# Performance work log

Hardware: AMD Instinct MI355X
Metric: run time of the kernel (lower is better)

The kernel has to match this reference:

```python
import jax, jax.numpy as jnp
import numpy as np

TEMPERATURE = 0.07
COS_EPS = 1e-8  # torch F.cosine_similarity clamps norms at eps=1e-8


def setup_inputs() -> dict:
    key = jax.random.key(0)
    features = jax.random.normal(key, (8192, 1024), dtype=jnp.float32)
    return {"features": features}


def reference(features):
    n = features.shape[0]
    b = n // 2
    # Cosine similarity as normalize + GEMM (equivalent to broadcasted F.cosine_similarity)
    norms = jnp.maximum(jnp.linalg.norm(features, axis=1, keepdims=True), COS_EPS)
    fn = features / norms                      # [N, D]
    sim = (fn @ fn.T) / TEMPERATURE            # [N, N]
    # Mask self-similarity on the diagonal with -inf
    diag = jnp.eye(n, dtype=bool)
    sim = jnp.where(diag, -jnp.inf, sim)
    # labels: positive of i is its paired augmentation (i+b mod n)
    labels = jnp.concatenate([jnp.arange(b) + b, jnp.arange(b)])  # [N]
    # Cross-entropy in one stable pass
    log_probs = jax.nn.log_softmax(sim, axis=1)
    loss = -jnp.mean(log_probs[jnp.arange(n), labels])
    return loss
```

## Files before the change

kernel.cpp:

```cpp
#include <hip/hip_runtime.h>
#include <hip/hip_bf16.h>

#define N_ROWS 8192
#define D_DIM  1024
#define HALF_N 4096
#define N_TILES 2080
constexpr float INV_T = 1.0f / 0.07f;

typedef __attribute__((ext_vector_type(4))) float f32x4;
typedef unsigned long u64;

__device__ __forceinline__ void async_ld16(const void* g, void* lds) {
    __builtin_amdgcn_global_load_lds(
        (const __attribute__((address_space(1))) void*)g,
        (__attribute__((address_space(3))) void*)lds,
        16, 0, 0);
}

__device__ __forceinline__ unsigned int pk_fp8x4(float a, float b, float c, float d) {
    int v = __builtin_amdgcn_cvt_pk_fp8_f32(a, b, 0, false);
    v = __builtin_amdgcn_cvt_pk_fp8_f32(c, d, v, true);
    return (unsigned int)v;
}

__global__ __launch_bounds__(256) void norm_kernel(const float* __restrict__ feat,
                                                   unsigned char* __restrict__ fn8,
                                                   float* __restrict__ row_sum,
                                                   float* __restrict__ s_target) {
    const int w = threadIdx.x >> 6, lane = threadIdx.x & 63;
    const int row = blockIdx.x * 4 + w;
    const int pair = (row + HALF_N) & (N_ROWS - 1);
    const float4* src = (const float4*)(feat + (size_t)row * D_DIM);
    const float4* psrc = (const float4*)(feat + (size_t)pair * D_DIM);
    float4 v[4];
    float ss = 0.f, sp = 0.f, dp = 0.f;
#pragma unroll
    for (int t = 0; t < 4; ++t) {
        v[t] = src[lane + 64 * t];
        float4 p = psrc[lane + 64 * t];
        ss += v[t].x * v[t].x + v[t].y * v[t].y + v[t].z * v[t].z + v[t].w * v[t].w;
        sp += p.x * p.x + p.y * p.y + p.z * p.z + p.w * p.w;
        dp += v[t].x * p.x + v[t].y * p.y + v[t].z * p.z + v[t].w * p.w;
    }
#pragma unroll
    for (int off = 32; off; off >>= 1) {
        ss += __shfl_xor(ss, off);
        sp += __shfl_xor(sp, off);
        dp += __shfl_xor(dp, off);
    }
    float nrm = fmaxf(sqrtf(ss), 1e-8f);
    if (lane == 0) {
        row_sum[row] = 0.f;
        s_target[row] = dp / (nrm * fmaxf(sqrtf(sp), 1e-8f)) * INV_T;
    }
    const float inv = 1.0f / nrm;
    unsigned int* dst = (unsigned int*)(fn8 + (size_t)row * D_DIM);
#pragma unroll
    for (int t = 0; t < 4; ++t)
        dst[lane + 64 * t] = pk_fp8x4(v[t].x * inv, v[t].y * inv, v[t].z * inv, v[t].w * inv);
}

__global__ __launch_bounds__(256) void simgemm_kernel(const unsigned char* __restrict__ fn8,
                                                      float* __restrict__ row_sum) {
    __shared__ __align__(16) unsigned char As[128 * 64];
    __shared__ __align__(16) unsigned char Bs[128 * 64];
    const int t = blockIdx.x;
    int a = (int)((sqrtf(8.f * (float)t + 1.f) - 1.f) * 0.5f);
    while ((a + 1) * (a + 2) / 2 <= t) ++a;
    while (a * (a + 1) / 2 > t) --a;
    const int I = t - a * (a + 1) / 2;
    const int J = a;
    const int r0 = I * 128, c0 = J * 128;
    const bool isdiag = (I == J);

    const int tid = threadIdx.x;
    const int w = tid >> 6, lane = tid & 63;
    const int q = lane >> 4, c16 = lane & 15;
    const int wr = (w >> 1) * 64;
    const int wc = (w & 1) * 64;
    const int wr4 = (w >> 1) * 4;
    const int wc4 = (w & 1) * 4;
    const int srow = lane >> 2;
    const int skoff = ((lane & 3) ^ ((srow >> 1) & 3)) * 16;
    const int fsw = (c16 >> 1) & 3;
    const int lbase = c16 * 64 + (q & 1) * 8;
    const int loff0 = lbase + (((q >> 1) + 0) ^ fsw) * 16;
    const int loff1 = lbase + (((q >> 1) + 2) ^ fsw) * 16;

    const unsigned char* pa0 = fn8 + (size_t)(r0 + w * 32 + srow) * D_DIM + skoff;
    const unsigned char* pa1 = pa0 + 16 * D_DIM;
    const unsigned char* pb0 = fn8 + (size_t)(c0 + w * 32 + srow) * D_DIM + skoff;
    const unsigned char* pb1 = pb0 + 16 * D_DIM;

    f32x4 acc[4][4];
#pragma unroll
    for (int i = 0; i < 4; ++i)
#pragma unroll
        for (int j = 0; j < 4; ++j) acc[i][j] = (f32x4){0.f, 0.f, 0.f, 0.f};

    for (int kt = 0; kt < 16; ++kt) {
        __syncthreads();
        async_ld16(pa0, (void*)&As[(w * 2 + 0) * 1024]);
        async_ld16(pa1, (void*)&As[(w * 2 + 1) * 1024]);
        async_ld16(pb0, (void*)&Bs[(w * 2 + 0) * 1024]);
        async_ld16(pb1, (void*)&Bs[(w * 2 + 1) * 1024]);
        pa0 += 64; pa1 += 64; pb0 += 64; pb1 += 64;
        __syncthreads();

        u64 a0[4], a1[4], b0[4], b1[4];
#pragma unroll
        for (int i = 0; i < 4; ++i) {
            a0[i] = *(const u64*)&As[(wr4 + i) * 1024 + loff0];
            a1[i] = *(const u64*)&As[(wr4 + i) * 1024 + loff1];
        }
#pragma unroll
        for (int j = 0; j < 4; ++j) {
            b0[j] = *(const u64*)&Bs[(wc4 + j) * 1024 + loff0];
            b1[j] = *(const u64*)&Bs[(wc4 + j) * 1024 + loff1];
        }
#pragma unroll
        for (int i = 0; i < 4; ++i)
#pragma unroll
            for (int j = 0; j < 4; ++j) {
                acc[i][j] = __builtin_amdgcn_mfma_f32_16x16x32_fp8_fp8(
                    (long)a0[i], (long)b0[j], acc[i][j], 0, 0, 0);
                acc[i][j] = __builtin_amdgcn_mfma_f32_16x16x32_fp8_fp8(
                    (long)a1[i], (long)b1[j], acc[i][j], 0, 0, 0);
            }
    }

    float cs[4] = {0.f, 0.f, 0.f, 0.f};
#pragma unroll
    for (int i = 0; i < 4; ++i) {
        const int growb = r0 + wr + i * 16 + q * 4;
#pragma unroll
        for (int r = 0; r < 4; ++r) {
            const int grow = growb + r;
            float s = 0.f;
#pragma unroll
            for (int j = 0; j < 4; ++j) {
                const int gcol = c0 + wc + j * 16 + c16;
                float sim = acc[i][j][r] * INV_T;
                float e = __expf(sim - INV_T);
                if (isdiag && grow == gcol) e = 0.f;
                s += e;
                cs[j] += e;
            }
            s += __shfl_xor(s, 1);
            s += __shfl_xor(s, 2);
            s += __shfl_xor(s, 4);
            s += __shfl_xor(s, 8);
            if (c16 == 0) atomicAdd(&row_sum[grow], s);
        }
    }
    if (!isdiag) {
#pragma unroll
        for (int j = 0; j < 4; ++j) {
            float s = cs[j];
            s += __shfl_xor(s, 16);
            s += __shfl_xor(s, 32);
            if (q == 0) atomicAdd(&row_sum[c0 + wc + j * 16 + c16], s);
        }
    }
}

__global__ __launch_bounds__(256) void loss_kernel(const float* __restrict__ row_sum,
                                                   const float* __restrict__ s_target,
                                                   float* __restrict__ out) {
    float local = 0.f;
    for (int i = threadIdx.x; i < N_ROWS; i += 256)
        local += (INV_T + __logf(row_sum[i])) - s_target[i];
#pragma unroll
    for (int off = 32; off; off >>= 1) local += __shfl_xor(local, off);
    __shared__ float part[4];
    if ((threadIdx.x & 63) == 0) part[threadIdx.x >> 6] = local;
    __syncthreads();
    if (threadIdx.x == 0)
        out[0] = (part[0] + part[1] + part[2] + part[3]) * (1.0f / N_ROWS);
}

extern "C" void kernel_launch(void* const* d_in, const int* in_sizes, int n_in,
                              void* d_out, int out_size, void* d_ws, size_t ws_size,
                              hipStream_t stream) {
    const float* feat = (const float*)d_in[0];
    float* out = (float*)d_out;
    char* ws = (char*)d_ws;

    unsigned char* fn8 = (unsigned char*)ws;
    size_t off = (size_t)N_ROWS * D_DIM;
    float* row_sum = (float*)(ws + off);   off += N_ROWS * sizeof(float);
    float* s_target = (float*)(ws + off);

    norm_kernel<<<N_ROWS / 4, 256, 0, stream>>>(feat, fn8, row_sum, s_target);
    simgemm_kernel<<<N_TILES, 256, 0, stream>>>(fn8, row_sum);
    loss_kernel<<<1, 256, 0, stream>>>(row_sum, s_target, out);
}
```

Baseline: 152.5 us.

## Fuse loss reduction into GEMM via last-block counter and take target logits from GEMM

The norm kernel no longer reads the paired row to compute the positive-pair similarity. The GEMM tiles on the J==I+32 block diagonal write those target logits directly from the fp8 accumulators. The separate loss kernel is removed: the last GEMM block to finish, found with an atomic done counter, performs the final log-sum reduction. This saves one launch and halves the norm kernel's global reads. In exchange the target logit now carries fp8 quantization error, and correctness depends on the relaxed atomic ordering between blocks.

```diff
diff --git a/kernel.cpp b/kernel.cpp
--- a/kernel.cpp
+++ b/kernel.cpp
@@ -26,33 +26,22 @@
 __global__ __launch_bounds__(256) void norm_kernel(const float* __restrict__ feat,
                                                    unsigned char* __restrict__ fn8,
                                                    float* __restrict__ row_sum,
-                                                   float* __restrict__ s_target) {
+                                                   unsigned int* __restrict__ done_cnt) {
     const int w = threadIdx.x >> 6, lane = threadIdx.x & 63;
     const int row = blockIdx.x * 4 + w;
-    const int pair = (row + HALF_N) & (N_ROWS - 1);
+    if (blockIdx.x == 0 && threadIdx.x == 0) *done_cnt = 0u;
     const float4* src = (const float4*)(feat + (size_t)row * D_DIM);
-    const float4* psrc = (const float4*)(feat + (size_t)pair * D_DIM);
     float4 v[4];
-    float ss = 0.f, sp = 0.f, dp = 0.f;
+    float ss = 0.f;
 #pragma unroll
     for (int t = 0; t < 4; ++t) {
         v[t] = src[lane + 64 * t];
-        float4 p = psrc[lane + 64 * t];
         ss += v[t].x * v[t].x + v[t].y * v[t].y + v[t].z * v[t].z + v[t].w * v[t].w;
-        sp += p.x * p.x + p.y * p.y + p.z * p.z + p.w * p.w;
-        dp += v[t].x * p.x + v[t].y * p.y + v[t].z * p.z + v[t].w * p.w;
-    }
-#pragma unroll
-    for (int off = 32; off; off >>= 1) {
-        ss += __shfl_xor(ss, off);
-        sp += __shfl_xor(sp, off);
-        dp += __shfl_xor(dp, off);
-    }
+    }
+#pragma unroll
+    for (int off = 32; off; off >>= 1) ss += __shfl_xor(ss, off);
     float nrm = fmaxf(sqrtf(ss), 1e-8f);
-    if (lane == 0) {
-        row_sum[row] = 0.f;
-        s_target[row] = dp / (nrm * fmaxf(sqrtf(sp), 1e-8f)) * INV_T;
-    }
+    if (lane == 0) row_sum[row] = 0.f;
     const float inv = 1.0f / nrm;
     unsigned int* dst = (unsigned int*)(fn8 + (size_t)row * D_DIM);
 #pragma unroll
@@ -61,7 +50,10 @@
 }
 
 __global__ __launch_bounds__(256) void simgemm_kernel(const unsigned char* __restrict__ fn8,
-                                                      float* __restrict__ row_sum) {
+                                                      float* __restrict__ row_sum,
+                                                      float* __restrict__ s_target,
+                                                      unsigned int* __restrict__ done_cnt,
+                                                      float* __restrict__ out) {
     __shared__ __align__(16) unsigned char As[128 * 64];
     __shared__ __align__(16) unsigned char Bs[128 * 64];
     const int t = blockIdx.x;
@@ -72,6 +64,7 @@
     const int J = a;
     const int r0 = I * 128, c0 = J * 128;
     const bool isdiag = (I == J);
+    const bool haspair = (J == I + 32);
 
     const int tid = threadIdx.x;
     const int w = tid >> 6, lane = tid & 63;
@@ -143,6 +136,12 @@
                 float sim = acc[i][j][r] * INV_T;
                 float e = __expf(sim - INV_T);
                 if (isdiag && grow == gcol) e = 0.f;
+                if (haspair && gcol == grow + HALF_N) {
+                    __hip_atomic_store(&s_target[grow], sim, __ATOMIC_RELAXED,
+                                       __HIP_MEMORY_SCOPE_AGENT);
+                    __hip_atomic_store(&s_target[gcol], sim, __ATOMIC_RELAXED,
+                                       __HIP_MEMORY_SCOPE_AGENT);
+                }
                 s += e;
                 cs[j] += e;
             }
@@ -162,21 +161,31 @@
             if (q == 0) atomicAdd(&row_sum[c0 + wc + j * 16 + c16], s);
         }
     }
-}
-
-__global__ __launch_bounds__(256) void loss_kernel(const float* __restrict__ row_sum,
-                                                   const float* __restrict__ s_target,
-                                                   float* __restrict__ out) {
-    float local = 0.f;
-    for (int i = threadIdx.x; i < N_ROWS; i += 256)
-        local += (INV_T + __logf(row_sum[i])) - s_target[i];
-#pragma unroll
-    for (int off = 32; off; off >>= 1) local += __shfl_xor(local, off);
-    __shared__ float part[4];
-    if ((threadIdx.x & 63) == 0) part[threadIdx.x >> 6] = local;
+
+    __builtin_amdgcn_s_waitcnt(0);
     __syncthreads();
-    if (threadIdx.x == 0)
-        out[0] = (part[0] + part[1] + part[2] + part[3]) * (1.0f / N_ROWS);
+    __shared__ unsigned int my_ord;
+    if (tid == 0)
+        my_ord = __hip_atomic_fetch_add(done_cnt, 1u, __ATOMIC_RELAXED,
+                                        __HIP_MEMORY_SCOPE_AGENT);
+    __syncthreads();
+    if (my_ord == N_TILES - 1) {
+        float local = 0.f;
+        for (int i = tid; i < N_ROWS; i += 256) {
+            float rsv = __hip_atomic_load(&row_sum[i], __ATOMIC_RELAXED,
+                                          __HIP_MEMORY_SCOPE_AGENT);
+            float stv = __hip_atomic_load(&s_target[i], __ATOMIC_RELAXED,
+                                          __HIP_MEMORY_SCOPE_AGENT);
+            local += (INV_T + __logf(rsv)) - stv;
+        }
+#pragma unroll
+        for (int off = 32; off; off >>= 1) local += __shfl_xor(local, off);
+        __shared__ float part[4];
+        if ((tid & 63) == 0) part[tid >> 6] = local;
+        __syncthreads();
+        if (tid == 0)
+            out[0] = (part[0] + part[1] + part[2] + part[3]) * (1.0f / N_ROWS);
+    }
 }
 
 extern "C" void kernel_launch(void* const* d_in, const int* in_sizes, int n_in,
@@ -189,9 +198,9 @@
     unsigned char* fn8 = (unsigned char*)ws;
     size_t off = (size_t)N_ROWS * D_DIM;
     float* row_sum = (float*)(ws + off);   off += N_ROWS * sizeof(float);
-    float* s_target = (float*)(ws + off);
-
-    norm_kernel<<<N_ROWS / 4, 256, 0, stream>>>(feat, fn8, row_sum, s_target);
-    simgemm_kernel<<<N_TILES, 256, 0, stream>>>(fn8, row_sum);
-    loss_kernel<<<1, 256, 0, stream>>>(row_sum, s_target, out);
-}
+    float* s_target = (float*)(ws + off);  off += N_ROWS * sizeof(float);
+    unsigned int* done_cnt = (unsigned int*)(ws + off);
+
+    norm_kernel<<<N_ROWS / 4, 256, 0, stream>>>(feat, fn8, row_sum, done_cnt);
+    simgemm_kernel<<<N_TILES, 256, 0, stream>>>(fn8, row_sum, s_target, done_cnt, out);
+}
```

Measured after the change: 155.4 us. No clear change (+1.9%).
